# Kernel optimization log

Hardware: AMD Instinct MI355X
Metric: run time of the kernel (lower is better)

The kernel has to match this reference:

```python
import jax, jax.numpy as jnp
from jax import lax
import numpy as np

WIN = 8          # window side -> N = 64 tokens per window
DIM = 256
HEADS = 8
B_ = 4096        # batch * num_windows
DN = ('NCHW', 'OIHW', 'NCHW')


def _rel_pos_index(win):
    ch = np.arange(win)
    coords = np.stack(np.meshgrid(ch, ch, indexing='ij'))
    flat = coords.reshape(2, -1)
    rel = flat[:, :, None] - flat[:, None, :]                      # [2,N,N]
    rel = rel.transpose(1, 2, 0).astype(np.int32)                  # [N,N,2]
    rel[..., 0] += win - 1
    rel[..., 1] += win - 1
    rel[..., 0] *= 2 * win - 1
    return rel.sum(-1)                                             # [N,N] in [0, (2w-1)^2)


def _sepconv(x, dw_w, dw_b, pw_w, pw_b):
    # x: [B,C,H,W]; depthwise 3x3 (groups=C) + bias + ReLU, then pointwise 1x1 + bias
    C = x.shape[1]
    y = lax.conv_general_dilated(x, dw_w, (1, 1), [(1, 1), (1, 1)],
                                 dimension_numbers=DN, feature_group_count=C)
    y = jax.nn.relu(y + dw_b[None, :, None, None])
    y = lax.conv_general_dilated(y, pw_w, (1, 1), [(0, 0), (0, 0)],
                                 dimension_numbers=DN)
    return y + pw_b[None, :, None, None]


def setup_inputs() -> dict:
    key = jax.random.key(0)
    ks = jax.random.split(key, 16)
    C = DIM
    d = {}
    d['x'] = jax.random.normal(ks[0], (B_, WIN * WIN, C), dtype=jnp.float32)
    for i, p in enumerate(['q', 'k', 'v']):
        d[f'{p}_dw_w'] = jax.random.normal(ks[1 + 4 * i], (C, 1, 3, 3), jnp.float32) * 0.05
        d[f'{p}_dw_b'] = jax.random.normal(ks[2 + 4 * i], (C,), jnp.float32) * 0.02
        d[f'{p}_pw_w'] = jax.random.normal(ks[3 + 4 * i], (C, C, 1, 1), jnp.float32) * 0.05
        d[f'{p}_pw_b'] = jax.random.normal(ks[4 + 4 * i], (C,), jnp.float32) * 0.02
    d['bias_table'] = jax.random.normal(ks[13], ((2 * WIN - 1) ** 2, HEADS), jnp.float32) * 0.02
    d['proj_w'] = jax.random.normal(ks[14], (C, C), jnp.float32) * 0.02
    d['proj_b'] = jax.random.normal(ks[15], (C,), jnp.float32) * 0.02
    d['rel_index'] = jnp.asarray(_rel_pos_index(WIN))  # [N,N] int32
    return d


def reference(x, q_dw_w, q_dw_b, q_pw_w, q_pw_b,
              k_dw_w, k_dw_b, k_pw_w, k_pw_b,
              v_dw_w, v_dw_b, v_pw_w, v_pw_b,
              bias_table, proj_w, proj_b, rel_index):
    B, N, C = x.shape
    H = HEADS
    dh = C // H
    scale = dh ** (-0.5)
    l = WIN
    xi = x.transpose(0, 2, 1).reshape(B, C, l, l)          # b (l w) c -> b c l w
    q = _sepconv(xi, q_dw_w, q_dw_b, q_pw_w, q_pw_b)
    k = _sepconv(xi, k_dw_w, k_dw_b, k_pw_w, k_pw_b)
    v = _sepconv(xi, v_dw_w, v_dw_b, v_pw_w, v_pw_b)
    # b (h d) l w -> b h (l w) d
    q = q.reshape(B, H, dh, N).transpose(0, 1, 3, 2)
    k = k.reshape(B, H, dh, N).transpose(0, 1, 3, 2)
    v = v.reshape(B, H, dh, N).transpose(0, 1, 3, 2)
    attn = jnp.einsum('bhnd,bhmd->bhnm', q * scale, k)     # [B,H,N,N]
    bias = bias_table[rel_index]                           # [N,N,H] gather
    attn = attn + bias.transpose(2, 0, 1)[None]            # ratio=1, repeat is identity
    attn = jax.nn.softmax(attn, axis=-1)
    out = jnp.einsum('bhnm,bhmd->bhnd', attn, v)           # [B,H,N,dh]
    out = out.transpose(0, 2, 1, 3).reshape(B, N, C)
    return out @ proj_w.T + proj_b
```

## Files before the change

### kernel.cpp

```cpp
#include <hip/hip_runtime.h>

typedef __attribute__((ext_vector_type(8))) short bf16x8;
typedef __attribute__((ext_vector_type(4))) float f32x4;

__device__ __forceinline__ float b2f(unsigned short u) {
  unsigned int v = ((unsigned int)u) << 16;
  return __builtin_bit_cast(float, v);
}
__device__ __forceinline__ unsigned short f2b(float f) {
  unsigned int v = __builtin_bit_cast(unsigned int, f);
  v += 0x7FFFu + ((v >> 16) & 1u);
  return (unsigned short)(v >> 16);
}

__global__ __launch_bounds__(512) void winattn_kernel(
    const float* __restrict__ xg,
    const float* __restrict__ dww0, const float* __restrict__ dwb0,
    const float* __restrict__ pww0, const float* __restrict__ pwb0,
    const float* __restrict__ dww1, const float* __restrict__ dwb1,
    const float* __restrict__ pww1, const float* __restrict__ pwb1,
    const float* __restrict__ dww2, const float* __restrict__ dwb2,
    const float* __restrict__ pww2, const float* __restrict__ pwb2,
    const float* __restrict__ bt,
    const float* __restrict__ pjw, const float* __restrict__ pjb,
    const int* __restrict__ rel,
    float* __restrict__ outg)
{
  __shared__ __align__(16) unsigned short smem[65536];
  unsigned short* sm0 = smem;
  unsigned short* sm1 = smem + 16384;
  unsigned short* sm2 = smem + 32768;
  unsigned short* sm3 = smem + 49152;

  const int tid  = threadIdx.x;
  const int lane = tid & 63;
  const int wv   = tid >> 6;
  const int lq   = lane >> 4;
  const int lc   = lane & 15;
  const int b    = blockIdx.x;

  const f32x4 zero4 = {0.f, 0.f, 0.f, 0.f};

  {
    const float4* gx = (const float4*)(xg + (size_t)b * 16384);
    ushort4* sx = (ushort4*)sm0;
#pragma unroll
    for (int i = 0; i < 8; ++i) {
      const float4 v = gx[tid + 512 * i];
      ushort4 u;
      u.x = f2b(v.x); u.y = f2b(v.y); u.z = f2b(v.z); u.w = f2b(v.w);
      sx[tid + 512 * i] = u;
    }
  }
  __syncthreads();

  const float* dwwA[3] = {dww0, dww1, dww2};
  const float* dwbA[3] = {dwb0, dwb1, dwb2};
  const float* pwwA[3] = {pww0, pww1, pww2};
  const float* pwbA[3] = {pwb0, pwb1, pwb2};

  const int cch = tid & 255;
  const int hlf = tid >> 8;

#pragma unroll
  for (int p = 0; p < 3; ++p) {
    {
      float w9[9];
#pragma unroll
      for (int t = 0; t < 9; ++t) w9[t] = dwwA[p][cch * 9 + t];
      const float bsv = dwbA[p][cch];
      const int l0 = hlf * 4;
      float row[3][8];
#pragma unroll
      for (int w = 0; w < 8; ++w)
        row[0][w] = (hlf == 0) ? 0.f : b2f(sm0[((l0 - 1) * 8 + w) * 256 + cch]);
#pragma unroll
      for (int w = 0; w < 8; ++w)
        row[1][w] = b2f(sm0[(l0 * 8 + w) * 256 + cch]);
#pragma unroll
      for (int li = 0; li < 4; ++li) {
        const int l = l0 + li;
        const bool haveNext = (l < 7);
#pragma unroll
        for (int w = 0; w < 8; ++w)
          row[2][w] = haveNext ? b2f(sm0[((l + 1) * 8 + w) * 256 + cch]) : 0.f;
#pragma unroll
        for (int w = 0; w < 8; ++w) {
          float acc = bsv;
#pragma unroll
          for (int dl = 0; dl < 3; ++dl) {
#pragma unroll
            for (int dc = 0; dc < 3; ++dc) {
              const int w2 = w + dc - 1;
              if (w2 >= 0 && w2 < 8) acc = fmaf(w9[dl * 3 + dc], row[dl][w2], acc);
            }
          }
          acc = fmaxf(acc, 0.f);
          const int n  = l * 8 + w;
          const int f  = (n >> 4) * 8 + (cch >> 5);
          const int lp = (n & 15) + 16 * ((cch & 31) >> 3);
          sm1[f * 512 + lp * 8 + (cch & 7)] = f2b(acc);
        }
#pragma unroll
        for (int w = 0; w < 8; ++w) { row[0][w] = row[1][w]; row[1][w] = row[2][w]; }
      }
    }
    __syncthreads();

    {
      const float* W = pwwA[p];
      f32x4 acc[4][2];
#pragma unroll
      for (int i = 0; i < 4; ++i)
#pragma unroll
        for (int t = 0; t < 2; ++t) acc[i][t] = zero4;
#pragma unroll
      for (int kk = 0; kk < 8; ++kk) {
        bf16x8 a[4], bb[2];
#pragma unroll
        for (int i = 0; i < 4; ++i)
          a[i] = *(const bf16x8*)&sm1[(i * 8 + kk) * 512 + lane * 8];
#pragma unroll
        for (int t = 0; t < 2; ++t) {
          const int co = 16 * (2 * wv + t) + lc;
          const float4* wp = (const float4*)(W + co * 256 + 32 * kk + 8 * lq);
          const float4 wa = wp[0];
          const float4 wc = wp[1];
          bf16x8 bv;
          bv[0] = (short)f2b(wa.x); bv[1] = (short)f2b(wa.y);
          bv[2] = (short)f2b(wa.z); bv[3] = (short)f2b(wa.w);
          bv[4] = (short)f2b(wc.x); bv[5] = (short)f2b(wc.y);
          bv[6] = (short)f2b(wc.z); bv[7] = (short)f2b(wc.w);
          bb[t] = bv;
        }
#pragma unroll
        for (int i = 0; i < 4; ++i)
#pragma unroll
          for (int t = 0; t < 2; ++t)
            acc[i][t] = __builtin_amdgcn_mfma_f32_16x16x32_bf16(a[i], bb[t], acc[i][t], 0, 0, 0);
      }
#pragma unroll
      for (int t = 0; t < 2; ++t) {
        const int co = 16 * (2 * wv + t) + lc;
        const float pb = pwbA[p][co];
#pragma unroll
        for (int i = 0; i < 4; ++i) {
#pragma unroll
          for (int r = 0; r < 4; ++r) {
            const float v = acc[i][t][r] + pb;
            const int n = 16 * i + 4 * lq + r;
            if (p < 2) {
              unsigned short* dst = (p == 0) ? sm2 : sm3;
              const int f  = i * 8 + (co >> 5);
              const int lp = (n & 15) + 16 * ((co & 31) >> 3);
              dst[f * 512 + lp * 8 + (co & 7)] = f2b(v);
            } else {
              const int h   = co >> 5;
              const int ct2 = (co >> 4) & 1;
              const int kt  = i >> 1;
              const int g   = (h * 2 + ct2) * 2 + kt;
              const int tl  = n & 31;
              const int lp  = (tl >> 3) * 16 + (co & 15);
              sm0[g * 512 + lp * 8 + (tl & 7)] = f2b(v);
            }
          }
        }
      }
    }
    __syncthreads();
  }

  float rsum[4][4];
  {
    const int h = wv;
    f32x4 s[4][4];
    {
      bf16x8 aq[4];
#pragma unroll
      for (int i = 0; i < 4; ++i)
        aq[i] = *(const bf16x8*)&sm2[(i * 8 + h) * 512 + lane * 8];
#pragma unroll
      for (int ct = 0; ct < 4; ++ct) {
        const bf16x8 bk = *(const bf16x8*)&sm3[(ct * 8 + h) * 512 + lane * 8];
#pragma unroll
        for (int i = 0; i < 4; ++i)
          s[i][ct] = __builtin_amdgcn_mfma_f32_16x16x32_bf16(aq[i], bk, zero4, 0, 0, 0);
      }
    }
    const float scale = 0.17677669529663687f;
#pragma unroll
    for (int i = 0; i < 4; ++i) {
#pragma unroll
      for (int r = 0; r < 4; ++r) {
        const int n = 16 * i + 4 * lq + r;
        const int* relrow = rel + n * 64;
#pragma unroll
        for (int ct = 0; ct < 4; ++ct) {
          const int m = 16 * ct + lc;
          const float bv = bt[relrow[m] * 8 + h];
          s[i][ct][r] = s[i][ct][r] * scale + bv;
        }
      }
    }
    float mx[4][4];
#pragma unroll
    for (int i = 0; i < 4; ++i) {
#pragma unroll
      for (int r = 0; r < 4; ++r) {
        float m0 = fmaxf(fmaxf(s[i][0][r], s[i][1][r]), fmaxf(s[i][2][r], s[i][3][r]));
        m0 = fmaxf(m0, __shfl_xor(m0, 1));
        m0 = fmaxf(m0, __shfl_xor(m0, 2));
        m0 = fmaxf(m0, __shfl_xor(m0, 4));
        m0 = fmaxf(m0, __shfl_xor(m0, 8));
        mx[i][r] = m0;
      }
    }
#pragma unroll
    for (int i = 0; i < 4; ++i) {
#pragma unroll
      for (int r = 0; r < 4; ++r) {
        float s0 = 0.f;
#pragma unroll
        for (int ct = 0; ct < 4; ++ct) {
          const float e = __expf(s[i][ct][r] - mx[i][r]);
          s[i][ct][r] = e;
          s0 += e;
        }
        s0 += __shfl_xor(s0, 1);
        s0 += __shfl_xor(s0, 2);
        s0 += __shfl_xor(s0, 4);
        s0 += __shfl_xor(s0, 8);
        rsum[i][r] = s0;
      }
    }
    f32x4 o[4][2];
#pragma unroll
    for (int i = 0; i < 4; ++i)
#pragma unroll
      for (int t = 0; t < 2; ++t) o[i][t] = zero4;
    unsigned short* Ppk = sm1 + wv * 2048;
#pragma unroll
    for (int kk = 0; kk < 2; ++kk) {
#pragma unroll
      for (int td = 0; td < 2; ++td) {
        const int ct = 2 * kk + td;
#pragma unroll
        for (int i = 0; i < 4; ++i) {
#pragma unroll
          for (int r = 0; r < 4; ++r) {
            const int np = 4 * lq + r;
            const int cm = 16 * td + lc;
            Ppk[i * 512 + (np + 16 * (cm >> 3)) * 8 + (cm & 7)] = f2b(s[i][ct][r]);
          }
        }
      }
      bf16x8 pa[4];
#pragma unroll
      for (int i = 0; i < 4; ++i)
        pa[i] = *(const bf16x8*)&Ppk[i * 512 + lane * 8];
#pragma unroll
      for (int ct2 = 0; ct2 < 2; ++ct2) {
        const bf16x8 vb = *(const bf16x8*)&sm0[((h * 2 + ct2) * 2 + kk) * 512 + lane * 8];
#pragma unroll
        for (int i = 0; i < 4; ++i)
          o[i][ct2] = __builtin_amdgcn_mfma_f32_16x16x32_bf16(pa[i], vb, o[i][ct2], 0, 0, 0);
      }
    }
#pragma unroll
    for (int ct2 = 0; ct2 < 2; ++ct2) {
#pragma unroll
      for (int i = 0; i < 4; ++i) {
#pragma unroll
        for (int r = 0; r < 4; ++r) {
          const float v = o[i][ct2][r] / rsum[i][r];
          const int np = 4 * lq + r;
          const int lp = np + 16 * (2 * ct2 + (lc >> 3));
          sm2[(i * 8 + h) * 512 + lp * 8 + (lc & 7)] = f2b(v);
        }
      }
    }
  }
  __syncthreads();

  {
    f32x4 acc[4][2];
#pragma unroll
    for (int i = 0; i < 4; ++i)
#pragma unroll
      for (int t = 0; t < 2; ++t) acc[i][t] = zero4;
#pragma unroll
    for (int kk = 0; kk < 8; ++kk) {
      bf16x8 a[4], bb[2];
#pragma unroll
      for (int i = 0; i < 4; ++i)
        a[i] = *(const bf16x8*)&sm2[(i * 8 + kk) * 512 + lane * 8];
#pragma unroll
      for (int t = 0; t < 2; ++t) {
        const int co = 16 * (2 * wv + t) + lc;
        const float4* wp = (const float4*)(pjw + co * 256 + 32 * kk + 8 * lq);
        const float4 wa = wp[0];
        const float4 wc = wp[1];
        bf16x8 bv;
        bv[0] = (short)f2b(wa.x); bv[1] = (short)f2b(wa.y);
        bv[2] = (short)f2b(wa.z); bv[3] = (short)f2b(wa.w);
        bv[4] = (short)f2b(wc.x); bv[5] = (short)f2b(wc.y);
        bv[6] = (short)f2b(wc.z); bv[7] = (short)f2b(wc.w);
        bb[t] = bv;
      }
#pragma unroll
      for (int i = 0; i < 4; ++i)
#pragma unroll
        for (int t = 0; t < 2; ++t)
          acc[i][t] = __builtin_amdgcn_mfma_f32_16x16x32_bf16(a[i], bb[t], acc[i][t], 0, 0, 0);
    }
    float* og = outg + (size_t)b * 16384;
#pragma unroll
    for (int t = 0; t < 2; ++t) {
      const int co = 16 * (2 * wv + t) + lc;
      const float pb = pjb[co];
#pragma unroll
      for (int i = 0; i < 4; ++i) {
#pragma unroll
        for (int r = 0; r < 4; ++r) {
          const int n = 16 * i + 4 * lq + r;
          og[n * 256 + co] = acc[i][t][r] + pb;
        }
      }
    }
  }
}

extern "C" void kernel_launch(void* const* d_in, const int* in_sizes, int n_in,
                              void* d_out, int out_size, void* d_ws, size_t ws_size,
                              hipStream_t stream) {
  (void)in_sizes; (void)n_in; (void)d_ws; (void)ws_size; (void)out_size;
  const float* x    = (const float*)d_in[0];
  const float* qdww = (const float*)d_in[1];
  const float* qdwb = (const float*)d_in[2];
  const float* qpww = (const float*)d_in[3];
  const float* qpwb = (const float*)d_in[4];
  const float* kdww = (const float*)d_in[5];
  const float* kdwb = (const float*)d_in[6];
  const float* kpww = (const float*)d_in[7];
  const float* kpwb = (const float*)d_in[8];
  const float* vdww = (const float*)d_in[9];
  const float* vdwb = (const float*)d_in[10];
  const float* vpww = (const float*)d_in[11];
  const float* vpwb = (const float*)d_in[12];
  const float* bt   = (const float*)d_in[13];
  const float* pjw  = (const float*)d_in[14];
  const float* pjb  = (const float*)d_in[15];
  const int* rel    = (const int*)d_in[16];
  float* out        = (float*)d_out;

  hipLaunchKernelGGL(winattn_kernel, dim3(4096), dim3(512), 0, stream,
                     x, qdww, qdwb, qpww, qpwb, kdww, kdwb, kpww, kpwb,
                     vdww, vdwb, vpww, vpwb, bt, pjw, pjb, rel, out);
}
```

Measured before the change: 899.0 us.

## Restructure window attention kernel with channel-sliced depthwise conv and swizzled LDS

Rewrites the fused kernel so depthwise conv reads x directly from global memory in fp32 vectors, with the depthwise weights staged once in LDS. The conv is processed in two 128-channel slices, so the intermediate buffer is halved. LDS buffers now use XOR-swizzled row layouts, and V fragments are kept in registers. Q and K are computed as transposed MFMAs, and softmax is done per row with cross-lane shuffles and a reciprocal instead of a division. The goal is fewer bank conflicts and less LDS staging. In exchange, LDS grows to 80KB, more barriers are added, and x is re-read from global memory for each of the three projections.

```diff
diff --git a/kernel.cpp b/kernel.cpp
--- a/kernel.cpp
+++ b/kernel.cpp
@@ -3,17 +3,27 @@
 typedef __attribute__((ext_vector_type(8))) short bf16x8;
 typedef __attribute__((ext_vector_type(4))) float f32x4;
 
-__device__ __forceinline__ float b2f(unsigned short u) {
-  unsigned int v = ((unsigned int)u) << 16;
-  return __builtin_bit_cast(float, v);
-}
+#define SLICE_B 0
+#define Q_B     16384
+#define K_B     49152
+#define DWB_OFF 27648
+
 __device__ __forceinline__ unsigned short f2b(float f) {
   unsigned int v = __builtin_bit_cast(unsigned int, f);
   v += 0x7FFFu + ((v >> 16) & 1u);
   return (unsigned short)(v >> 16);
 }
-
-__global__ __launch_bounds__(512) void winattn_kernel(
+__device__ __forceinline__ unsigned int pk2(float a, float b) {
+  return (unsigned int)f2b(a) | ((unsigned int)f2b(b) << 16);
+}
+__device__ __forceinline__ bf16x8 pack8(const float4& a, const float4& b) {
+  union { unsigned int u[4]; bf16x8 v; } x;
+  x.u[0] = pk2(a.x, a.y); x.u[1] = pk2(a.z, a.w);
+  x.u[2] = pk2(b.x, b.y); x.u[3] = pk2(b.z, b.w);
+  return x.v;
+}
+
+__global__ __launch_bounds__(512, 4) void winattn_kernel(
     const float* __restrict__ xg,
     const float* __restrict__ dww0, const float* __restrict__ dwb0,
     const float* __restrict__ pww0, const float* __restrict__ pwb0,
@@ -26,306 +36,305 @@
     const int* __restrict__ rel,
     float* __restrict__ outg)
 {
-  __shared__ __align__(16) unsigned short smem[65536];
-  unsigned short* sm0 = smem;
-  unsigned short* sm1 = smem + 16384;
-  unsigned short* sm2 = smem + 32768;
-  unsigned short* sm3 = smem + 49152;
+  __shared__ __align__(16) unsigned char smem[81920];
 
   const int tid  = threadIdx.x;
   const int lane = tid & 63;
   const int wv   = tid >> 6;
-  const int lq   = lane >> 4;
   const int lc   = lane & 15;
+  const int lq2  = lane >> 4;
   const int b    = blockIdx.x;
-
-  const f32x4 zero4 = {0.f, 0.f, 0.f, 0.f};
-
-  {
-    const float4* gx = (const float4*)(xg + (size_t)b * 16384);
-    ushort4* sx = (ushort4*)sm0;
-#pragma unroll
-    for (int i = 0; i < 8; ++i) {
-      const float4 v = gx[tid + 512 * i];
-      ushort4 u;
-      u.x = f2b(v.x); u.y = f2b(v.y); u.z = f2b(v.z); u.w = f2b(v.w);
-      sx[tid + 512 * i] = u;
-    }
-  }
-  __syncthreads();
+  const float* xb = xg + (size_t)b * 16384;
 
   const float* dwwA[3] = {dww0, dww1, dww2};
   const float* dwbA[3] = {dwb0, dwb1, dwb2};
   const float* pwwA[3] = {pww0, pww1, pww2};
   const float* pwbA[3] = {pwb0, pwb1, pwb2};
 
-  const int cch = tid & 255;
-  const int hlf = tid >> 8;
-
-#pragma unroll
-  for (int p = 0; p < 3; ++p) {
-    {
-      float w9[9];
-#pragma unroll
-      for (int t = 0; t < 9; ++t) w9[t] = dwwA[p][cch * 9 + t];
-      const float bsv = dwbA[p][cch];
-      const int l0 = hlf * 4;
-      float row[3][8];
-#pragma unroll
-      for (int w = 0; w < 8; ++w)
-        row[0][w] = (hlf == 0) ? 0.f : b2f(sm0[((l0 - 1) * 8 + w) * 256 + cch]);
-#pragma unroll
-      for (int w = 0; w < 8; ++w)
-        row[1][w] = b2f(sm0[(l0 * 8 + w) * 256 + cch]);
-#pragma unroll
-      for (int li = 0; li < 4; ++li) {
-        const int l = l0 + li;
-        const bool haveNext = (l < 7);
-#pragma unroll
-        for (int w = 0; w < 8; ++w)
-          row[2][w] = haveNext ? b2f(sm0[((l + 1) * 8 + w) * 256 + cch]) : 0.f;
-#pragma unroll
-        for (int w = 0; w < 8; ++w) {
-          float acc = bsv;
-#pragma unroll
-          for (int dl = 0; dl < 3; ++dl) {
-#pragma unroll
-            for (int dc = 0; dc < 3; ++dc) {
-              const int w2 = w + dc - 1;
-              if (w2 >= 0 && w2 < 8) acc = fmaf(w9[dl * 3 + dc], row[dl][w2], acc);
-            }
+  const f32x4 zero4 = {0.f, 0.f, 0.f, 0.f};
+
+  for (int idx = tid; idx < 6912; idx += 512) {
+    const int p = idx / 2304, rem = idx % 2304;
+    const int c = rem / 9, tap = rem % 9;
+    *(float*)(smem + K_B + (((p * 9 + tap) * 256) + c) * 4) = dwwA[p][c * 9 + tap];
+  }
+  for (int idx = tid; idx < 768; idx += 512) {
+    const int p = idx >> 8, c = idx & 255;
+    *(float*)(smem + K_B + DWB_OFF + (p * 256 + c) * 4) = dwbA[p][c];
+  }
+  __syncthreads();
+
+  auto dwconv = [&](int p, int s) {
+    const int c8 = tid & 15;
+    const int strip = tid >> 4;
+    const int l = strip >> 2, w0 = (strip & 3) * 2;
+    const int n0 = l * 8 + w0;
+#pragma unroll
+    for (int h4 = 0; h4 < 2; ++h4) {
+      const int cb = s * 128 + c8 * 8 + h4 * 4;
+      f32x4 o0 = *(const f32x4*)(smem + K_B + DWB_OFF + (p * 256 + cb) * 4);
+      f32x4 o1 = o0;
+#pragma unroll
+      for (int dl = 0; dl < 3; ++dl) {
+        const int row = l + dl - 1;
+        const bool rok = (row >= 0) && (row < 8);
+        f32x4 xv[4];
+#pragma unroll
+        for (int wn = 0; wn < 4; ++wn) {
+          const int col = w0 + wn - 1;
+          f32x4 z = zero4;
+          if (rok && col >= 0 && col < 8)
+            z = *(const f32x4*)(xb + (row * 8 + col) * 256 + cb);
+          xv[wn] = z;
+        }
+#pragma unroll
+        for (int dc = 0; dc < 3; ++dc) {
+          const f32x4 wt = *(const f32x4*)(smem + K_B + (((p * 9 + dl * 3 + dc) * 256) + cb) * 4);
+#pragma unroll
+          for (int j = 0; j < 4; ++j) {
+            o0[j] = fmaf(wt[j], xv[dc][j], o0[j]);
+            o1[j] = fmaf(wt[j], xv[dc + 1][j], o1[j]);
           }
-          acc = fmaxf(acc, 0.f);
-          const int n  = l * 8 + w;
-          const int f  = (n >> 4) * 8 + (cch >> 5);
-          const int lp = (n & 15) + 16 * ((cch & 31) >> 3);
-          sm1[f * 512 + lp * 8 + (cch & 7)] = f2b(acc);
-        }
-#pragma unroll
-        for (int w = 0; w < 8; ++w) { row[0][w] = row[1][w]; row[1][w] = row[2][w]; }
-      }
-    }
-    __syncthreads();
-
-    {
-      const float* W = pwwA[p];
-      f32x4 acc[4][2];
-#pragma unroll
-      for (int i = 0; i < 4; ++i)
-#pragma unroll
-        for (int t = 0; t < 2; ++t) acc[i][t] = zero4;
-#pragma unroll
-      for (int kk = 0; kk < 8; ++kk) {
-        bf16x8 a[4], bb[2];
-#pragma unroll
-        for (int i = 0; i < 4; ++i)
-          a[i] = *(const bf16x8*)&sm1[(i * 8 + kk) * 512 + lane * 8];
+        }
+      }
+#pragma unroll
+      for (int j = 0; j < 4; ++j) { o0[j] = fmaxf(o0[j], 0.f); o1[j] = fmaxf(o1[j], 0.f); }
+      uint2 u0; u0.x = pk2(o0[0], o0[1]); u0.y = pk2(o0[2], o0[3]);
+      uint2 u1; u1.x = pk2(o1[0], o1[1]); u1.y = pk2(o1[2], o1[3]);
+      const int n1 = n0 + 1;
+      *(uint2*)(smem + SLICE_B + n0 * 256 + ((c8 ^ (n0 & 15)) & 15) * 16 + h4 * 8) = u0;
+      *(uint2*)(smem + SLICE_B + n1 * 256 + ((c8 ^ (n1 & 15)) & 15) * 16 + h4 * 8) = u1;
+    }
+  };
+
+  bf16x8 vfrag[2][2];
+  {
+    f32x4 av[4][2];
+#pragma unroll
+    for (int i = 0; i < 4; ++i)
+#pragma unroll
+      for (int t = 0; t < 2; ++t) av[i][t] = zero4;
+
+    for (int s = 0; s < 2; ++s) {
+      dwconv(2, s);
+      __syncthreads();
+      const float* W = pwwA[2];
+#pragma unroll
+      for (int kk = 0; kk < 4; ++kk) {
+        bf16x8 afr[4];
+#pragma unroll
+        for (int i = 0; i < 4; ++i) {
+          const int m = 16 * i + lc;
+          const int s8 = 4 * kk + lq2;
+          afr[i] = *(const bf16x8*)(smem + SLICE_B + m * 256 + ((s8 ^ (m & 15)) & 15) * 16);
+        }
+        bf16x8 bb[2];
 #pragma unroll
         for (int t = 0; t < 2; ++t) {
           const int co = 16 * (2 * wv + t) + lc;
-          const float4* wp = (const float4*)(W + co * 256 + 32 * kk + 8 * lq);
-          const float4 wa = wp[0];
-          const float4 wc = wp[1];
-          bf16x8 bv;
-          bv[0] = (short)f2b(wa.x); bv[1] = (short)f2b(wa.y);
-          bv[2] = (short)f2b(wa.z); bv[3] = (short)f2b(wa.w);
-          bv[4] = (short)f2b(wc.x); bv[5] = (short)f2b(wc.y);
-          bv[6] = (short)f2b(wc.z); bv[7] = (short)f2b(wc.w);
-          bb[t] = bv;
+          const int ci0 = s * 128 + 32 * kk + 8 * lq2;
+          const float4 wa = *(const float4*)(W + co * 256 + ci0);
+          const float4 wb = *(const float4*)(W + co * 256 + ci0 + 4);
+          bb[t] = pack8(wa, wb);
         }
 #pragma unroll
         for (int i = 0; i < 4; ++i)
 #pragma unroll
           for (int t = 0; t < 2; ++t)
-            acc[i][t] = __builtin_amdgcn_mfma_f32_16x16x32_bf16(a[i], bb[t], acc[i][t], 0, 0, 0);
-      }
+            av[i][t] = __builtin_amdgcn_mfma_f32_16x16x32_bf16(afr[i], bb[t], av[i][t], 0, 0, 0);
+      }
+      __syncthreads();
+    }
+#pragma unroll
+    for (int t = 0; t < 2; ++t) {
+      const float pb = pwbA[2][16 * (2 * wv + t) + lc];
+      const int c_local = 16 * t + lc;
+#pragma unroll
+      for (int i = 0; i < 4; ++i) {
+        const int m0 = 16 * i + 4 * lq2;
+        const float v0 = av[i][t][0] + pb, v1 = av[i][t][1] + pb;
+        const float v2 = av[i][t][2] + pb, v3 = av[i][t][3] + pb;
+        uint2 u; u.x = pk2(v0, v1); u.y = pk2(v2, v3);
+        *(uint2*)(smem + Q_B + wv * 4096 + c_local * 128 +
+                  (((m0 >> 3) ^ (c_local & 7)) & 7) * 16 + (lq2 & 1) * 8) = u;
+      }
+    }
+#pragma unroll
+    for (int ct = 0; ct < 2; ++ct)
+#pragma unroll
+      for (int kk = 0; kk < 2; ++kk) {
+        const int c_local = 16 * ct + lc;
+        const int s8 = 4 * kk + lq2;
+        vfrag[ct][kk] = *(const bf16x8*)(smem + Q_B + wv * 4096 + c_local * 128 +
+                                         ((s8 ^ (c_local & 7)) & 7) * 16);
+      }
+  }
+
+  for (int qk = 0; qk < 2; ++qk) {
+    const int dstB = qk ? K_B : Q_B;
+    f32x4 acc[2][4];
+#pragma unroll
+    for (int cot = 0; cot < 2; ++cot)
+#pragma unroll
+      for (int nt = 0; nt < 4; ++nt) acc[cot][nt] = zero4;
+
+    for (int s = 0; s < 2; ++s) {
+      dwconv(qk, s);
+      __syncthreads();
+      const float* W = pwwA[qk];
+#pragma unroll
+      for (int kk = 0; kk < 4; ++kk) {
+        bf16x8 afrW[2];
+#pragma unroll
+        for (int cot = 0; cot < 2; ++cot) {
+          const int co = 32 * wv + 16 * cot + lc;
+          const int ci0 = s * 128 + 32 * kk + 8 * lq2;
+          const float4 wa = *(const float4*)(W + co * 256 + ci0);
+          const float4 wb = *(const float4*)(W + co * 256 + ci0 + 4);
+          afrW[cot] = pack8(wa, wb);
+        }
+        bf16x8 bfr[4];
+#pragma unroll
+        for (int nt = 0; nt < 4; ++nt) {
+          const int n = 16 * nt + lc;
+          const int s8 = 4 * kk + lq2;
+          bfr[nt] = *(const bf16x8*)(smem + SLICE_B + n * 256 + ((s8 ^ (n & 15)) & 15) * 16);
+        }
+#pragma unroll
+        for (int cot = 0; cot < 2; ++cot)
+#pragma unroll
+          for (int nt = 0; nt < 4; ++nt)
+            acc[cot][nt] = __builtin_amdgcn_mfma_f32_16x16x32_bf16(afrW[cot], bfr[nt], acc[cot][nt], 0, 0, 0);
+      }
+      __syncthreads();
+    }
+#pragma unroll
+    for (int cot = 0; cot < 2; ++cot) {
+      const int c0 = 32 * wv + 16 * cot + 4 * lq2;
+      float pb[4];
+#pragma unroll
+      for (int r = 0; r < 4; ++r) pb[r] = pwbA[qk][c0 + r];
+#pragma unroll
+      for (int nt = 0; nt < 4; ++nt) {
+        const int n = 16 * nt + lc;
+        const float v0 = acc[cot][nt][0] + pb[0], v1 = acc[cot][nt][1] + pb[1];
+        const float v2 = acc[cot][nt][2] + pb[2], v3 = acc[cot][nt][3] + pb[3];
+        uint2 u; u.x = pk2(v0, v1); u.y = pk2(v2, v3);
+        *(uint2*)(smem + dstB + n * 512 + (((c0 >> 3) ^ (n & 31)) & 31) * 16 + (lq2 & 1) * 8) = u;
+      }
+    }
+  }
+
+  {
+    const int h = wv;
+    bf16x8 kfrag[4];
+#pragma unroll
+    for (int mt = 0; mt < 4; ++mt) {
+      const int m = 16 * mt + lc;
+      kfrag[mt] = *(const bf16x8*)(smem + K_B + m * 512 + (((4 * h + lq2) ^ (m & 31)) & 31) * 16);
+    }
+    const float scale = 0.17677669529663687f;
+#pragma unroll
+    for (int qt = 0; qt < 4; ++qt) {
+      const int n = 16 * qt + lc;
+      const bf16x8 qfrag = *(const bf16x8*)(smem + Q_B + n * 512 + (((4 * h + lq2) ^ (n & 31)) & 31) * 16);
+      f32x4 sc[4];
+#pragma unroll
+      for (int mt = 0; mt < 4; ++mt)
+        sc[mt] = __builtin_amdgcn_mfma_f32_16x16x32_bf16(kfrag[mt], qfrag, zero4, 0, 0, 0);
+      const int* relrow = rel + n * 64;
+      float sv[4][4];
+#pragma unroll
+      for (int mt = 0; mt < 4; ++mt)
+#pragma unroll
+        for (int r = 0; r < 4; ++r) {
+          const int m = 16 * mt + 4 * lq2 + r;
+          sv[mt][r] = sc[mt][r] * scale + bt[relrow[m] * 8 + h];
+        }
+      float mx = sv[0][0];
+#pragma unroll
+      for (int mt = 0; mt < 4; ++mt)
+#pragma unroll
+        for (int r = 0; r < 4; ++r) mx = fmaxf(mx, sv[mt][r]);
+      mx = fmaxf(mx, __shfl_xor(mx, 16));
+      mx = fmaxf(mx, __shfl_xor(mx, 32));
+      float sum = 0.f;
+#pragma unroll
+      for (int mt = 0; mt < 4; ++mt)
+#pragma unroll
+        for (int r = 0; r < 4; ++r) {
+          sv[mt][r] = __expf(sv[mt][r] - mx);
+          sum += sv[mt][r];
+        }
+      sum += __shfl_xor(sum, 16);
+      sum += __shfl_xor(sum, 32);
+      const float rinv = __builtin_amdgcn_rcpf(sum);
+#pragma unroll
+      for (int mt = 0; mt < 4; ++mt) {
+        const int m0 = 16 * mt + 4 * lq2;
+        uint2 u; u.x = pk2(sv[mt][0], sv[mt][1]); u.y = pk2(sv[mt][2], sv[mt][3]);
+        *(uint2*)(smem + SLICE_B + wv * 2048 + lc * 128 +
+                  (((m0 >> 3) ^ (lc & 7)) & 7) * 16 + (lq2 & 1) * 8) = u;
+      }
+      f32x4 o[2] = {zero4, zero4};
+#pragma unroll
+      for (int kk = 0; kk < 2; ++kk) {
+        const bf16x8 pf = *(const bf16x8*)(smem + SLICE_B + wv * 2048 + lc * 128 +
+                                           (((4 * kk + lq2) ^ (lc & 7)) & 7) * 16);
+#pragma unroll
+        for (int ct = 0; ct < 2; ++ct)
+          o[ct] = __builtin_amdgcn_mfma_f32_16x16x32_bf16(vfrag[ct][kk], pf, o[ct], 0, 0, 0);
+      }
+#pragma unroll
+      for (int ct = 0; ct < 2; ++ct) {
+        const int c0 = 32 * h + 16 * ct + 4 * lq2;
+        const float v0 = o[ct][0] * rinv, v1 = o[ct][1] * rinv;
+        const float v2 = o[ct][2] * rinv, v3 = o[ct][3] * rinv;
+        uint2 u; u.x = pk2(v0, v1); u.y = pk2(v2, v3);
+        *(uint2*)(smem + K_B + n * 512 + (((c0 >> 3) ^ (n & 31)) & 31) * 16 + (lq2 & 1) * 8) = u;
+      }
+    }
+  }
+  __syncthreads();
+
+  {
+    f32x4 pacc[4][2];
+#pragma unroll
+    for (int i = 0; i < 4; ++i)
+#pragma unroll
+      for (int t = 0; t < 2; ++t) pacc[i][t] = zero4;
+#pragma unroll
+    for (int kk = 0; kk < 8; ++kk) {
+      bf16x8 afr[4];
+#pragma unroll
+      for (int i = 0; i < 4; ++i) {
+        const int n = 16 * i + lc;
+        afr[i] = *(const bf16x8*)(smem + K_B + n * 512 + (((4 * kk + lq2) ^ (n & 31)) & 31) * 16);
+      }
+      bf16x8 bb[2];
 #pragma unroll
       for (int t = 0; t < 2; ++t) {
         const int co = 16 * (2 * wv + t) + lc;
-        const float pb = pwbA[p][co];
-#pragma unroll
-        for (int i = 0; i < 4; ++i) {
-#pragma unroll
-          for (int r = 0; r < 4; ++r) {
-            const float v = acc[i][t][r] + pb;
-            const int n = 16 * i + 4 * lq + r;
-            if (p < 2) {
-              unsigned short* dst = (p == 0) ? sm2 : sm3;
-              const int f  = i * 8 + (co >> 5);
-              const int lp = (n & 15) + 16 * ((co & 31) >> 3);
-              dst[f * 512 + lp * 8 + (co & 7)] = f2b(v);
-            } else {
-              const int h   = co >> 5;
-              const int ct2 = (co >> 4) & 1;
-              const int kt  = i >> 1;
-              const int g   = (h * 2 + ct2) * 2 + kt;
-              const int tl  = n & 31;
-              const int lp  = (tl >> 3) * 16 + (co & 15);
-              sm0[g * 512 + lp * 8 + (tl & 7)] = f2b(v);
-            }
-          }
-        }
-      }
-    }
-    __syncthreads();
-  }
-
-  float rsum[4][4];
-  {
-    const int h = wv;
-    f32x4 s[4][4];
-    {
-      bf16x8 aq[4];
+        const float4 wa = *(const float4*)(pjw + co * 256 + 32 * kk + 8 * lq2);
+        const float4 wb = *(const float4*)(pjw + co * 256 + 32 * kk + 8 * lq2 + 4);
+        bb[t] = pack8(wa, wb);
+      }
 #pragma unroll
       for (int i = 0; i < 4; ++i)
-        aq[i] = *(const bf16x8*)&sm2[(i * 8 + h) * 512 + lane * 8];
-#pragma unroll
-      for (int ct = 0; ct < 4; ++ct) {
-        const bf16x8 bk = *(const bf16x8*)&sm3[(ct * 8 + h) * 512 + lane * 8];
-#pragma unroll
-        for (int i = 0; i < 4; ++i)
-          s[i][ct] = __builtin_amdgcn_mfma_f32_16x16x32_bf16(aq[i], bk, zero4, 0, 0, 0);
-      }
-    }
-    const float scale = 0.17677669529663687f;
-#pragma unroll
-    for (int i = 0; i < 4; ++i) {
-#pragma unroll
-      for (int r = 0; r < 4; ++r) {
-        const int n = 16 * i + 4 * lq + r;
-        const int* relrow = rel + n * 64;
-#pragma unroll
-        for (int ct = 0; ct < 4; ++ct) {
-          const int m = 16 * ct + lc;
-          const float bv = bt[relrow[m] * 8 + h];
-          s[i][ct][r] = s[i][ct][r] * scale + bv;
-        }
-      }
-    }
-    float mx[4][4];
-#pragma unroll
-    for (int i = 0; i < 4; ++i) {
-#pragma unroll
-      for (int r = 0; r < 4; ++r) {
-        float m0 = fmaxf(fmaxf(s[i][0][r], s[i][1][r]), fmaxf(s[i][2][r], s[i][3][r]));
-        m0 = fmaxf(m0, __shfl_xor(m0, 1));
-        m0 = fmaxf(m0, __shfl_xor(m0, 2));
-        m0 = fmaxf(m0, __shfl_xor(m0, 4));
-        m0 = fmaxf(m0, __shfl_xor(m0, 8));
-        mx[i][r] = m0;
-      }
-    }
-#pragma unroll
-    for (int i = 0; i < 4; ++i) {
-#pragma unroll
-      for (int r = 0; r < 4; ++r) {
-        float s0 = 0.f;
-#pragma unroll
-        for (int ct = 0; ct < 4; ++ct) {
-          const float e = __expf(s[i][ct][r] - mx[i][r]);
-          s[i][ct][r] = e;
-          s0 += e;
-        }
-        s0 += __shfl_xor(s0, 1);
-        s0 += __shfl_xor(s0, 2);
-        s0 += __shfl_xor(s0, 4);
-        s0 += __shfl_xor(s0, 8);
-        rsum[i][r] = s0;
-      }
-    }
-    f32x4 o[4][2];
-#pragma unroll
-    for (int i = 0; i < 4; ++i)
-#pragma unroll
-      for (int t = 0; t < 2; ++t) o[i][t] = zero4;
-    unsigned short* Ppk = sm1 + wv * 2048;
-#pragma unroll
-    for (int kk = 0; kk < 2; ++kk) {
-#pragma unroll
-      for (int td = 0; td < 2; ++td) {
-        const int ct = 2 * kk + td;
-#pragma unroll
-        for (int i = 0; i < 4; ++i) {
-#pragma unroll
-          for (int r = 0; r < 4; ++r) {
-            const int np = 4 * lq + r;
-            const int cm = 16 * td + lc;
-            Ppk[i * 512 + (np + 16 * (cm >> 3)) * 8 + (cm & 7)] = f2b(s[i][ct][r]);
-          }
-        }
-      }
-      bf16x8 pa[4];
-#pragma unroll
-      for (int i = 0; i < 4; ++i)
-        pa[i] = *(const bf16x8*)&Ppk[i * 512 + lane * 8];
-#pragma unroll
-      for (int ct2 = 0; ct2 < 2; ++ct2) {
-        const bf16x8 vb = *(const bf16x8*)&sm0[((h * 2 + ct2) * 2 + kk) * 512 + lane * 8];
-#pragma unroll
-        for (int i = 0; i < 4; ++i)
-          o[i][ct2] = __builtin_amdgcn_mfma_f32_16x16x32_bf16(pa[i], vb, o[i][ct2], 0, 0, 0);
-      }
-    }
-#pragma unroll
-    for (int ct2 = 0; ct2 < 2; ++ct2) {
-#pragma unroll
-      for (int i = 0; i < 4; ++i) {
-#pragma unroll
-        for (int r = 0; r < 4; ++r) {
-          const float v = o[i][ct2][r] / rsum[i][r];
-          const int np = 4 * lq + r;
-          const int lp = np + 16 * (2 * ct2 + (lc >> 3));
-          sm2[(i * 8 + h) * 512 + lp * 8 + (lc & 7)] = f2b(v);
-        }
-      }
-    }
-  }
-  __syncthreads();
-
-  {
-    f32x4 acc[4][2];
-#pragma unroll
-    for (int i = 0; i < 4; ++i)
-#pragma unroll
-      for (int t = 0; t < 2; ++t) acc[i][t] = zero4;
-#pragma unroll
-    for (int kk = 0; kk < 8; ++kk) {
-      bf16x8 a[4], bb[2];
-#pragma unroll
-      for (int i = 0; i < 4; ++i)
-        a[i] = *(const bf16x8*)&sm2[(i * 8 + kk) * 512 + lane * 8];
-#pragma unroll
-      for (int t = 0; t < 2; ++t) {
-        const int co = 16 * (2 * wv + t) + lc;
-        const float4* wp = (const float4*)(pjw + co * 256 + 32 * kk + 8 * lq);
-        const float4 wa = wp[0];
-        const float4 wc = wp[1];
-        bf16x8 bv;
-        bv[0] = (short)f2b(wa.x); bv[1] = (short)f2b(wa.y);
-        bv[2] = (short)f2b(wa.z); bv[3] = (short)f2b(wa.w);
-        bv[4] = (short)f2b(wc.x); bv[5] = (short)f2b(wc.y);
-        bv[6] = (short)f2b(wc.z); bv[7] = (short)f2b(wc.w);
-        bb[t] = bv;
-      }
-#pragma unroll
-      for (int i = 0; i < 4; ++i)
 #pragma unroll
         for (int t = 0; t < 2; ++t)
-          acc[i][t] = __builtin_amdgcn_mfma_f32_16x16x32_bf16(a[i], bb[t], acc[i][t], 0, 0, 0);
+          pacc[i][t] = __builtin_amdgcn_mfma_f32_16x16x32_bf16(afr[i], bb[t], pacc[i][t], 0, 0, 0);
     }
     float* og = outg + (size_t)b * 16384;
 #pragma unroll
     for (int t = 0; t < 2; ++t) {
       const int co = 16 * (2 * wv + t) + lc;
-      const float pb = pjb[co];
-#pragma unroll
-      for (int i = 0; i < 4; ++i) {
-#pragma unroll
-        for (int r = 0; r < 4; ++r) {
-          const int n = 16 * i + 4 * lq + r;
-          og[n * 256 + co] = acc[i][t][r] + pb;
-        }
-      }
+      const float pbv = pjb[co];
+#pragma unroll
+      for (int i = 0; i < 4; ++i)
+#pragma unroll
+        for (int r = 0; r < 4; ++r)
+          og[(16 * i + 4 * lq2 + r) * 256 + co] = pacc[i][t][r] + pbv;
     }
   }
 }
```

New measurement: 1.591 ms. 1.77x slower.
